# Kernel tuning notes

Measured on AMD Instinct MI355X. Metric: run time of the kernel, lower is better.

Reference implementation:

```python
import jax, jax.numpy as jnp
import numpy as np

N_NODES = 100000
N_EDGES = 3200000
N_FEAT = 128
N_GRAPHS = 256


def setup_inputs() -> dict:
    key = jax.random.key(0)
    ks = jax.random.split(key, 12)
    x = jax.random.normal(ks[0], (N_NODES, N_FEAT), dtype=jnp.float32)
    edge_index = jax.random.randint(ks[1], (2, N_EDGES), 0, N_NODES, dtype=jnp.int64)
    edge_weight = jax.random.uniform(ks[2], (N_EDGES,), dtype=jnp.float32)
    batch = jnp.sort(jax.random.randint(ks[3], (N_NODES,), 0, N_GRAPHS, dtype=jnp.int64))
    def glorot(k, shape):
        lim = np.sqrt(6.0 / (shape[0] + shape[1]))
        return jax.random.uniform(k, shape, dtype=jnp.float32, minval=-lim, maxval=lim)
    W1 = glorot(ks[4], (N_FEAT, 64))
    b1 = jnp.zeros((64,), dtype=jnp.float32)
    W2 = glorot(ks[5], (64, 32))
    b2 = jnp.zeros((32,), dtype=jnp.float32)
    Wl1 = glorot(ks[6], (32, 16))
    bl1 = jnp.zeros((16,), dtype=jnp.float32)
    Wl2 = glorot(ks[7], (16, 1))
    bl2 = jnp.zeros((1,), dtype=jnp.float32)
    return {"x": x, "edge_index": edge_index, "edge_weight": edge_weight,
            "batch": batch, "W1": W1, "b1": b1, "W2": W2, "b2": b2,
            "Wl1": Wl1, "bl1": bl1, "Wl2": Wl2, "bl2": bl2}


def gcn_conv(x, row, col, ew, W, b, num_nodes):
    # x' = D^-1/2 (A + I) D^-1/2 (x W) + b, weights on edges, self-loop weight 1
    h = x @ W  # [N, out]
    deg = jax.ops.segment_sum(ew, col, num_segments=num_nodes) + 1.0  # self-loops add 1
    dinv = jnp.where(deg > 0, jax.lax.rsqrt(deg), 0.0)
    norm = dinv[row] * ew * dinv[col]  # [E]
    msg = h[row] * norm[:, None]  # edge-wise gather + scale
    agg = jax.ops.segment_sum(msg, col, num_segments=num_nodes)
    agg = agg + h * (dinv * dinv)[:, None]  # self-loop contribution
    return agg + b


def reference(x, edge_index, edge_weight, batch, W1, b1, W2, b2, Wl1, bl1, Wl2, bl2):
    row, col = edge_index[0], edge_index[1]
    h = jax.nn.relu(gcn_conv(x, row, col, edge_weight, W1, b1, N_NODES))
    # dropout is identity in eval mode
    h = gcn_conv(h, row, col, edge_weight, W2, b2, N_NODES)
    u = jax.ops.segment_sum(h, batch, num_segments=N_GRAPHS)  # global_add_pool
    out = jax.nn.relu(u @ Wl1 + bl1)
    out = out @ Wl2 + bl2
    return out.reshape(-1)
```

## Files before the change

kernel.cpp:

```cpp
#include <hip/hip_runtime.h>
#include <hip/hip_bf16.h>

#define N_NODES 100000
#define N_EDGES 3200000
#define N_GRAPHS 256

#define NBUCK 391
#define SORT_ITEMS 8192
#define NB_SORT ((N_EDGES + SORT_ITEMS - 1) / SORT_ITEMS)
#define HIST_N (NBUCK * NB_SORT)
#define ROW_MASK 131071

__device__ __forceinline__ float bfl(int d) {
    return __uint_as_float(((unsigned)d) << 16);
}
__device__ __forceinline__ float bfh(int d) {
    return __uint_as_float(((unsigned)d) & 0xffff0000u);
}
__device__ __forceinline__ unsigned short f2bf(float f) {
    __hip_bfloat16 b = __float2bfloat16(f);
    return *(unsigned short*)&b;
}

__global__ __launch_bounds__(512) void hist_kernel(const int* __restrict__ col,
                                                   int* __restrict__ hist) {
    __shared__ int h[NBUCK];
    int tid = threadIdx.x;
    for (int i = tid; i < NBUCK; i += 512) h[i] = 0;
    __syncthreads();
    int base = blockIdx.x * SORT_ITEMS + tid * 4;
    #pragma unroll
    for (int l = 0; l < SORT_ITEMS / 2048; ++l) {
        int e = base + l * 2048;
        if (e < N_EDGES) {
            int4 c4 = *(const int4*)&col[e];
            atomicAdd(&h[c4.x >> 8], 1);
            atomicAdd(&h[c4.y >> 8], 1);
            atomicAdd(&h[c4.z >> 8], 1);
            atomicAdd(&h[c4.w >> 8], 1);
        }
    }
    __syncthreads();
    for (int i = tid; i < NBUCK; i += 512) hist[i * NB_SORT + blockIdx.x] = h[i];
}

__global__ __launch_bounds__(256) void scanA_kernel(int* __restrict__ a,
                                                    int* __restrict__ bsum, int n) {
    __shared__ int s[256];
    int tid = threadIdx.x;
    int base = blockIdx.x * 4096 + tid * 16;
    int v[16];
    int sum = 0;
    #pragma unroll
    for (int i = 0; i < 16; ++i) { v[i] = (base + i < n) ? a[base + i] : 0; sum += v[i]; }
    s[tid] = sum;
    __syncthreads();
    for (int d = 1; d < 256; d <<= 1) {
        int x = (tid >= d) ? s[tid - d] : 0;
        __syncthreads();
        s[tid] += x;
        __syncthreads();
    }
    int run = s[tid] - sum;
    #pragma unroll
    for (int i = 0; i < 16; ++i) {
        if (base + i < n) a[base + i] = run;
        run += v[i];
    }
    if (tid == 255) bsum[blockIdx.x] = s[255];
}

__global__ __launch_bounds__(256) void scanB_kernel(int* bsum, int nb) {
    __shared__ int s[256];
    int tid = threadIdx.x;
    int v = (tid < nb) ? bsum[tid] : 0;
    s[tid] = v;
    __syncthreads();
    for (int d = 1; d < 256; d <<= 1) {
        int x = (tid >= d) ? s[tid - d] : 0;
        __syncthreads();
        s[tid] += x;
        __syncthreads();
    }
    if (tid < nb) bsum[tid] = s[tid] - v;
}

__global__ __launch_bounds__(512) void scatter_sort_kernel(const int* __restrict__ col,
                                                           const int* __restrict__ row,
                                                           const float* __restrict__ ew,
                                                           const int* __restrict__ hist,
                                                           const int* __restrict__ bsum,
                                                           int2* __restrict__ rw2) {
    __shared__ int offs[NBUCK];
    int tid = threadIdx.x;
    for (int i = tid; i < NBUCK; i += 512) {
        int idx = i * NB_SORT + blockIdx.x;
        offs[i] = hist[idx] + bsum[idx >> 12];
    }
    __syncthreads();
    int base = blockIdx.x * SORT_ITEMS + tid * 4;
    #pragma unroll
    for (int l = 0; l < SORT_ITEMS / 2048; ++l) {
        int e = base + l * 2048;
        if (e < N_EDGES) {
            int4 c4 = *(const int4*)&col[e];
            int4 r4 = *(const int4*)&row[e];
            float4 w4 = *(const float4*)&ew[e];
            int p0 = atomicAdd(&offs[c4.x >> 8], 1);
            int p1 = atomicAdd(&offs[c4.y >> 8], 1);
            int p2 = atomicAdd(&offs[c4.z >> 8], 1);
            int p3 = atomicAdd(&offs[c4.w >> 8], 1);
            int2 v0; v0.x = r4.x | ((c4.x & 255) << 17); v0.y = __float_as_int(w4.x);
            int2 v1; v1.x = r4.y | ((c4.y & 255) << 17); v1.y = __float_as_int(w4.y);
            int2 v2; v2.x = r4.z | ((c4.z & 255) << 17); v2.y = __float_as_int(w4.z);
            int2 v3; v3.x = r4.w | ((c4.w & 255) << 17); v3.y = __float_as_int(w4.w);
            rw2[p0] = v0;
            rw2[p1] = v1;
            rw2[p2] = v2;
            rw2[p3] = v3;
        }
    }
}

__global__ __launch_bounds__(256) void build_kernel(const int* __restrict__ hist,
                                                    const int* __restrict__ bsum,
                                                    const int2* __restrict__ rw2,
                                                    int* __restrict__ off,
                                                    int* __restrict__ cnt,
                                                    float* __restrict__ dinv,
                                                    int2* __restrict__ csr) {
    int b = blockIdx.x;
    int tid = threadIdx.x;
    int ib = b * NB_SORT;
    int begin = hist[ib] + bsum[ib >> 12];
    int end = N_EDGES;
    if (b + 1 < NBUCK) {
        int ie = (b + 1) * NB_SORT;
        end = hist[ie] + bsum[ie >> 12];
    }
    __shared__ int lcnt[256];
    __shared__ float ldeg[256];
    __shared__ int s[256];
    __shared__ int curo[256];
    lcnt[tid] = 0;
    ldeg[tid] = 0.f;
    __syncthreads();
    for (int e = begin + tid; e < end; e += 1024) {
        int2 a0 = rw2[e];
        int e1 = e + 256, e2 = e + 512, e3 = e + 768;
        int2 a1 = (e1 < end) ? rw2[e1] : make_int2(0, 0);
        int2 a2 = (e2 < end) ? rw2[e2] : make_int2(0, 0);
        int2 a3 = (e3 < end) ? rw2[e3] : make_int2(0, 0);
        atomicAdd(&lcnt[a0.x >> 17], 1);
        atomicAdd(&ldeg[a0.x >> 17], __int_as_float(a0.y));
        if (e1 < end) { atomicAdd(&lcnt[a1.x >> 17], 1); atomicAdd(&ldeg[a1.x >> 17], __int_as_float(a1.y)); }
        if (e2 < end) { atomicAdd(&lcnt[a2.x >> 17], 1); atomicAdd(&ldeg[a2.x >> 17], __int_as_float(a2.y)); }
        if (e3 < end) { atomicAdd(&lcnt[a3.x >> 17], 1); atomicAdd(&ldeg[a3.x >> 17], __int_as_float(a3.y)); }
    }
    __syncthreads();
    int v = lcnt[tid];
    s[tid] = v;
    __syncthreads();
    for (int d = 1; d < 256; d <<= 1) {
        int x = (tid >= d) ? s[tid - d] : 0;
        __syncthreads();
        s[tid] += x;
        __syncthreads();
    }
    int excl = s[tid] - v;
    int node = (b << 8) + tid;
    if (node < N_NODES) {
        off[node] = begin + excl;
        cnt[node] = v;
        dinv[node] = rsqrtf(1.0f + ldeg[tid]);
    }
    curo[tid] = begin + excl;
    __syncthreads();
    for (int e = begin + tid; e < end; e += 1024) {
        int2 a0 = rw2[e];
        int e1 = e + 256, e2 = e + 512, e3 = e + 768;
        int2 a1 = (e1 < end) ? rw2[e1] : make_int2(0, 0);
        int2 a2 = (e2 < end) ? rw2[e2] : make_int2(0, 0);
        int2 a3 = (e3 < end) ? rw2[e3] : make_int2(0, 0);
        int p0 = atomicAdd(&curo[a0.x >> 17], 1);
        csr[p0] = make_int2(a0.x & ROW_MASK, a0.y);
        if (e1 < end) { int p = atomicAdd(&curo[a1.x >> 17], 1); csr[p] = make_int2(a1.x & ROW_MASK, a1.y); }
        if (e2 < end) { int p = atomicAdd(&curo[a2.x >> 17], 1); csr[p] = make_int2(a2.x & ROW_MASK, a2.y); }
        if (e3 < end) { int p = atomicAdd(&curo[a3.x >> 17], 1); csr[p] = make_int2(a3.x & ROW_MASK, a3.y); }
    }
}

template <int IN, int OUT, int ROWS>
__global__ __launch_bounds__(256) void gemm_bf16_kernel(const float* __restrict__ X,
                                                        const float* __restrict__ W,
                                                        const float* __restrict__ scale,
                                                        unsigned short* __restrict__ H, int n) {
    constexpr int BK = 16;
    constexpr int TX = OUT / 4;
    constexpr int TY = ROWS / 8;
    static_assert(TX * TY == 256, "block must be 256 threads");
    __shared__ float xsT[BK][ROWS + 4];
    __shared__ float ws[BK][OUT + 4];
    int tid = threadIdx.x;
    int tx = tid % TX, ty = tid / TX;
    int r0 = blockIdx.x * ROWS;
    float acc[8][4] = {};
    for (int k0 = 0; k0 < IN; k0 += BK) {
        constexpr int XL = (ROWS * BK) / (256 * 4);
        #pragma unroll
        for (int l = 0; l < XL; ++l) {
            int t = tid + l * 256;
            int rr = t >> 2;
            int kp = (t & 3) * 4;
            float4 v = make_float4(0.f, 0.f, 0.f, 0.f);
            int gr = r0 + rr;
            if (gr < n) v = *(const float4*)&X[(size_t)gr * IN + k0 + kp];
            xsT[kp + 0][rr] = v.x;
            xsT[kp + 1][rr] = v.y;
            xsT[kp + 2][rr] = v.z;
            xsT[kp + 3][rr] = v.w;
        }
        constexpr int WL = (BK * OUT) / 4;
        if (WL == 256 || tid < WL) {
            int kr = tid / TX;
            int cp = (tid % TX) * 4;
            float4 v = *(const float4*)&W[(size_t)(k0 + kr) * OUT + cp];
            *(float4*)&ws[kr][cp] = v;
        }
        __syncthreads();
        #pragma unroll
        for (int kk = 0; kk < BK; ++kk) {
            float4 a0 = *(const float4*)&xsT[kk][ty * 8];
            float4 a1 = *(const float4*)&xsT[kk][ty * 8 + 4];
            float4 b = *(const float4*)&ws[kk][tx * 4];
            float av[8] = {a0.x, a0.y, a0.z, a0.w, a1.x, a1.y, a1.z, a1.w};
            float bv[4] = {b.x, b.y, b.z, b.w};
            #pragma unroll
            for (int i = 0; i < 8; ++i) {
                #pragma unroll
                for (int j = 0; j < 4; ++j) acc[i][j] = fmaf(av[i], bv[j], acc[i][j]);
            }
        }
        __syncthreads();
    }
    #pragma unroll
    for (int i = 0; i < 8; ++i) {
        int gr = r0 + ty * 8 + i;
        if (gr < n) {
            float sc = scale[gr];
            ushort4 o;
            o.x = f2bf(acc[i][0] * sc);
            o.y = f2bf(acc[i][1] * sc);
            o.z = f2bf(acc[i][2] * sc);
            o.w = f2bf(acc[i][3] * sc);
            *(ushort4*)&H[(size_t)gr * OUT + tx * 4] = o;
        }
    }
}

__global__ __launch_bounds__(256) void agg1_kernel(const int2* __restrict__ csr,
                                                   const int* __restrict__ off,
                                                   const int* __restrict__ cnt,
                                                   const float* __restrict__ dinv,
                                                   const unsigned short* __restrict__ h1t,
                                                   const float* __restrict__ b1,
                                                   float* __restrict__ h1p) {
    int lane = threadIdx.x & 63;
    int node = blockIdx.x * 4 + (threadIdx.x >> 6);
    int es = lane >> 3;
    int fb = lane & 7;
    int s = off[node], c = cnt[node];
    float acc[8] = {};
    for (int j0 = 0; j0 < c; j0 += 64) {
        int m = min(64, c - j0);
        int2 e = make_int2(0, 0);
        if (lane < m) e = csr[s + j0 + lane];
        int ng = (m + 7) >> 3;
        int g = 0;
        for (; g + 2 <= ng; g += 2) {
            int s0 = g * 8 + es;
            int s1 = s0 + 8;
            int r0 = __shfl(e.x, s0);
            float w0 = __int_as_float(__shfl(e.y, s0));
            int r1 = __shfl(e.x, s1);
            float w1 = __int_as_float(__shfl(e.y, s1));
            int4 d0 = *(const int4*)(h1t + (((size_t)r0) << 6) + (fb << 3));
            int4 d1 = *(const int4*)(h1t + (((size_t)r1) << 6) + (fb << 3));
            acc[0] = fmaf(w0, bfl(d0.x), acc[0]);
            acc[1] = fmaf(w0, bfh(d0.x), acc[1]);
            acc[2] = fmaf(w0, bfl(d0.y), acc[2]);
            acc[3] = fmaf(w0, bfh(d0.y), acc[3]);
            acc[4] = fmaf(w0, bfl(d0.z), acc[4]);
            acc[5] = fmaf(w0, bfh(d0.z), acc[5]);
            acc[6] = fmaf(w0, bfl(d0.w), acc[6]);
            acc[7] = fmaf(w0, bfh(d0.w), acc[7]);
            acc[0] = fmaf(w1, bfl(d1.x), acc[0]);
            acc[1] = fmaf(w1, bfh(d1.x), acc[1]);
            acc[2] = fmaf(w1, bfl(d1.y), acc[2]);
            acc[3] = fmaf(w1, bfh(d1.y), acc[3]);
            acc[4] = fmaf(w1, bfl(d1.z), acc[4]);
            acc[5] = fmaf(w1, bfh(d1.z), acc[5]);
            acc[6] = fmaf(w1, bfl(d1.w), acc[6]);
            acc[7] = fmaf(w1, bfh(d1.w), acc[7]);
        }
        if (g < ng) {
            int s0 = g * 8 + es;
            int r0 = __shfl(e.x, s0);
            float w0 = __int_as_float(__shfl(e.y, s0));
            int4 d0 = *(const int4*)(h1t + (((size_t)r0) << 6) + (fb << 3));
            acc[0] = fmaf(w0, bfl(d0.x), acc[0]);
            acc[1] = fmaf(w0, bfh(d0.x), acc[1]);
            acc[2] = fmaf(w0, bfl(d0.y), acc[2]);
            acc[3] = fmaf(w0, bfh(d0.y), acc[3]);
            acc[4] = fmaf(w0, bfl(d0.z), acc[4]);
            acc[5] = fmaf(w0, bfh(d0.z), acc[5]);
            acc[6] = fmaf(w0, bfl(d0.w), acc[6]);
            acc[7] = fmaf(w0, bfh(d0.w), acc[7]);
        }
    }
    #pragma unroll
    for (int mask = 8; mask <= 32; mask <<= 1) {
        #pragma unroll
        for (int k = 0; k < 8; ++k) acc[k] += __shfl_xor(acc[k], mask);
    }
    if (es == 0) {
        float di = dinv[node];
        int4 ds = *(const int4*)(h1t + (((size_t)node) << 6) + (fb << 3));
        float4 bv0 = *(const float4*)&b1[fb * 8];
        float4 bv1 = *(const float4*)&b1[fb * 8 + 4];
        float4 o0, o1;
        o0.x = fmaxf(fmaf(acc[0] + bfl(ds.x), di, bv0.x), 0.f);
        o0.y = fmaxf(fmaf(acc[1] + bfh(ds.x), di, bv0.y), 0.f);
        o0.z = fmaxf(fmaf(acc[2] + bfl(ds.y), di, bv0.z), 0.f);
        o0.w = fmaxf(fmaf(acc[3] + bfh(ds.y), di, bv0.w), 0.f);
        o1.x = fmaxf(fmaf(acc[4] + bfl(ds.z), di, bv1.x), 0.f);
        o1.y = fmaxf(fmaf(acc[5] + bfh(ds.z), di, bv1.y), 0.f);
        o1.z = fmaxf(fmaf(acc[6] + bfl(ds.w), di, bv1.z), 0.f);
        o1.w = fmaxf(fmaf(acc[7] + bfh(ds.w), di, bv1.w), 0.f);
        float* po = h1p + (size_t)node * 64 + fb * 8;
        *(float4*)po = o0;
        *(float4*)(po + 4) = o1;
    }
}

__global__ __launch_bounds__(256) void agg2_kernel(const int2* __restrict__ csr,
                                                   const int* __restrict__ off,
                                                   const int* __restrict__ cnt,
                                                   const float* __restrict__ dinv,
                                                   const unsigned short* __restrict__ h2t,
                                                   const float* __restrict__ b2,
                                                   float* __restrict__ h2p) {
    int lane = threadIdx.x & 63;
    int half = lane >> 5;
    int hl = lane & 31;
    int es = hl >> 2;
    int fb = hl & 3;
    int wid = threadIdx.x >> 6;
    int node = blockIdx.x * 8 + wid * 2 + half;
    int s = off[node], c = cnt[node];
    int lbase = half << 5;
    float acc[8] = {};
    for (int j0 = 0; j0 < c; j0 += 32) {
        int m = min(32, c - j0);
        int2 e = make_int2(0, 0);
        if (hl < m) e = csr[s + j0 + hl];
        int ng = (m + 7) >> 3;
        int g = 0;
        for (; g + 2 <= ng; g += 2) {
            int s0 = lbase + g * 8 + es;
            int s1 = s0 + 8;
            int r0 = __shfl(e.x, s0);
            float w0 = __int_as_float(__shfl(e.y, s0));
            int r1 = __shfl(e.x, s1);
            float w1 = __int_as_float(__shfl(e.y, s1));
            int4 d0 = *(const int4*)(h2t + (((size_t)r0) << 5) + (fb << 3));
            int4 d1 = *(const int4*)(h2t + (((size_t)r1) << 5) + (fb << 3));
            acc[0] = fmaf(w0, bfl(d0.x), acc[0]);
            acc[1] = fmaf(w0, bfh(d0.x), acc[1]);
            acc[2] = fmaf(w0, bfl(d0.y), acc[2]);
            acc[3] = fmaf(w0, bfh(d0.y), acc[3]);
            acc[4] = fmaf(w0, bfl(d0.z), acc[4]);
            acc[5] = fmaf(w0, bfh(d0.z), acc[5]);
            acc[6] = fmaf(w0, bfl(d0.w), acc[6]);
            acc[7] = fmaf(w0, bfh(d0.w), acc[7]);
            acc[0] = fmaf(w1, bfl(d1.x), acc[0]);
            acc[1] = fmaf(w1, bfh(d1.x), acc[1]);
            acc[2] = fmaf(w1, bfl(d1.y), acc[2]);
            acc[3] = fmaf(w1, bfh(d1.y), acc[3]);
            acc[4] = fmaf(w1, bfl(d1.z), acc[4]);
            acc[5] = fmaf(w1, bfh(d1.z), acc[5]);
            acc[6] = fmaf(w1, bfl(d1.w), acc[6]);
            acc[7] = fmaf(w1, bfh(d1.w), acc[7]);
        }
        if (g < ng) {
            int s0 = lbase + g * 8 + es;
            int r0 = __shfl(e.x, s0);
            float w0 = __int_as_float(__shfl(e.y, s0));
            int4 d0 = *(const int4*)(h2t + (((size_t)r0) << 5) + (fb << 3));
            acc[0] = fmaf(w0, bfl(d0.x), acc[0]);
            acc[1] = fmaf(w0, bfh(d0.x), acc[1]);
            acc[2] = fmaf(w0, bfl(d0.y), acc[2]);
            acc[3] = fmaf(w0, bfh(d0.y), acc[3]);
            acc[4] = fmaf(w0, bfl(d0.z), acc[4]);
            acc[5] = fmaf(w0, bfh(d0.z), acc[5]);
            acc[6] = fmaf(w0, bfl(d0.w), acc[6]);
            acc[7] = fmaf(w0, bfh(d0.w), acc[7]);
        }
    }
    #pragma unroll
    for (int mask = 4; mask <= 16; mask <<= 1) {
        #pragma unroll
        for (int k = 0; k < 8; ++k) acc[k] += __shfl_xor(acc[k], mask);
    }
    if (es == 0) {
        float di = dinv[node];
        int4 ds = *(const int4*)(h2t + (((size_t)node) << 5) + (fb << 3));
        float4 bv0 = *(const float4*)&b2[fb * 8];
        float4 bv1 = *(const float4*)&b2[fb * 8 + 4];
        float4 o0, o1;
        o0.x = fmaf(acc[0] + bfl(ds.x), di, bv0.x);
        o0.y = fmaf(acc[1] + bfh(ds.x), di, bv0.y);
        o0.z = fmaf(acc[2] + bfl(ds.y), di, bv0.z);
        o0.w = fmaf(acc[3] + bfh(ds.y), di, bv0.w);
        o1.x = fmaf(acc[4] + bfl(ds.z), di, bv1.x);
        o1.y = fmaf(acc[5] + bfh(ds.z), di, bv1.y);
        o1.z = fmaf(acc[6] + bfl(ds.w), di, bv1.z);
        o1.w = fmaf(acc[7] + bfh(ds.w), di, bv1.w);
        float* po = h2p + (size_t)node * 32 + fb * 8;
        *(float4*)po = o0;
        *(float4*)(po + 4) = o1;
    }
}

__global__ __launch_bounds__(256) void pool_kernel(const float* __restrict__ h2p,
                                                   const int* __restrict__ batch,
                                                   float* __restrict__ u) {
    int g = blockIdx.x;
    int lo = 0, hi = N_NODES;
    while (lo < hi) { int m = (lo + hi) >> 1; if (batch[m] < g) lo = m + 1; else hi = m; }
    int start = lo;
    hi = N_NODES;
    while (lo < hi) { int m = (lo + hi) >> 1; if (batch[m] < g + 1) lo = m + 1; else hi = m; }
    int end = lo;
    int f = threadIdx.x & 31, grp = threadIdx.x >> 5;
    float acc = 0.f;
    for (int n = start + grp; n < end; n += 8) acc += h2p[(size_t)n * 32 + f];
    __shared__ float red[8][32];
    red[grp][f] = acc;
    __syncthreads();
    if (threadIdx.x < 32) {
        float sum = 0.f;
        #pragma unroll
        for (int k = 0; k < 8; ++k) sum += red[k][threadIdx.x];
        u[g * 32 + threadIdx.x] = sum;
    }
}

__global__ __launch_bounds__(256) void head_kernel(const float* __restrict__ u,
                                                   const float* __restrict__ Wl1,
                                                   const float* __restrict__ bl1,
                                                   const float* __restrict__ Wl2,
                                                   const float* __restrict__ bl2,
                                                   float* __restrict__ out) {
    int g = threadIdx.x;
    float uu[32];
    #pragma unroll
    for (int k = 0; k < 32; ++k) uu[k] = u[g * 32 + k];
    float o = bl2[0];
    #pragma unroll
    for (int j = 0; j < 16; ++j) {
        float h = bl1[j];
        #pragma unroll
        for (int k = 0; k < 32; ++k) h = fmaf(uu[k], Wl1[k * 16 + j], h);
        o = fmaf(fmaxf(h, 0.f), Wl2[j], o);
    }
    out[g] = o;
}

extern "C" void kernel_launch(void* const* d_in, const int* in_sizes, int n_in,
                              void* d_out, int out_size, void* d_ws, size_t ws_size,
                              hipStream_t stream) {
    const float* x     = (const float*)d_in[0];
    const int*   ei    = (const int*)d_in[1];
    const float* ew    = (const float*)d_in[2];
    const int*   batch = (const int*)d_in[3];
    const float* W1    = (const float*)d_in[4];
    const float* b1    = (const float*)d_in[5];
    const float* W2    = (const float*)d_in[6];
    const float* b2    = (const float*)d_in[7];
    const float* Wl1   = (const float*)d_in[8];
    const float* bl1   = (const float*)d_in[9];
    const float* Wl2   = (const float*)d_in[10];
    const float* bl2   = (const float*)d_in[11];
    float* out = (float*)d_out;

    const int* row = ei;
    const int* col = ei + N_EDGES;

    char* p = (char*)d_ws;
    auto alloc = [&](size_t bytes) {
        char* q = p;
        p += (bytes + 255) & ~(size_t)255;
        return q;
    };
    int*   hist   = (int*)alloc((size_t)HIST_N * 4);
    int*   bsum   = (int*)alloc(1024 * 4);
    int2*  rw2    = (int2*)alloc((size_t)N_EDGES * 8);
    int*   off    = (int*)alloc(N_NODES * 4);
    int*   cnt    = (int*)alloc(N_NODES * 4);
    float* dinv   = (float*)alloc(N_NODES * 4);
    int2*  csr    = (int2*)alloc((size_t)N_EDGES * 8);
    unsigned short* h1t = (unsigned short*)rw2;
    float* h1p    = (float*)alloc((size_t)N_NODES * 64 * 4);
    unsigned short* h2t = (unsigned short*)alloc((size_t)N_NODES * 32 * 2);
    float* h2p    = (float*)alloc((size_t)N_NODES * 32 * 4);
    float* u      = (float*)alloc(N_GRAPHS * 32 * 4);

    const int nbScan = (HIST_N + 4095) / 4096;

    hist_kernel<<<NB_SORT, 512, 0, stream>>>(col, hist);
    scanA_kernel<<<nbScan, 256, 0, stream>>>(hist, bsum, HIST_N);
    scanB_kernel<<<1, 256, 0, stream>>>(bsum, nbScan);
    scatter_sort_kernel<<<NB_SORT, 512, 0, stream>>>(col, row, ew, hist, bsum, rw2);
    build_kernel<<<NBUCK, 256, 0, stream>>>(hist, bsum, rw2, off, cnt, dinv, csr);

    gemm_bf16_kernel<128, 64, 128><<<(N_NODES + 127) / 128, 256, 0, stream>>>(x, W1, dinv, h1t, N_NODES);
    agg1_kernel<<<N_NODES / 4, 256, 0, stream>>>(csr, off, cnt, dinv, h1t, b1, h1p);
    gemm_bf16_kernel<64, 32, 256><<<(N_NODES + 255) / 256, 256, 0, stream>>>(h1p, W2, dinv, h2t, N_NODES);
    agg2_kernel<<<N_NODES / 8, 256, 0, stream>>>(csr, off, cnt, dinv, h2t, b2, h2p);
    pool_kernel<<<N_GRAPHS, 256, 0, stream>>>(h2p, batch, u);
    head_kernel<<<1, 256, 0, stream>>>(u, Wl1, bl1, Wl2, bl2, out);
}
```

Measured before the change: 246.1 us.

## Store layer-1 output in bf16 and widen build kernel to 512 threads

The first aggregation kernel now writes its ReLU output as packed bf16 instead of fp32, and a new GEMM variant reads bf16 input and expands it to float in shared memory. This halves the bytes written by agg1 and read by the second GEMM. Separately, the CSR build kernel runs with 512 threads per bucket, with the scan widened to 512 and only the first 256 threads writing per-node outputs. Rounding layer-1 activations to bf16 adds a small precision loss before the second layer.

```diff
diff --git a/kernel.cpp b/kernel.cpp
--- a/kernel.cpp
+++ b/kernel.cpp
@@ -20,6 +20,9 @@
 __device__ __forceinline__ unsigned short f2bf(float f) {
     __hip_bfloat16 b = __float2bfloat16(f);
     return *(unsigned short*)&b;
+}
+__device__ __forceinline__ unsigned pack2bf(float lo, float hi) {
+    return (unsigned)f2bf(lo) | ((unsigned)f2bf(hi) << 16);
 }
 
 __global__ __launch_bounds__(512) void hist_kernel(const int* __restrict__ col,
@@ -122,7 +125,7 @@
     }
 }
 
-__global__ __launch_bounds__(256) void build_kernel(const int* __restrict__ hist,
+__global__ __launch_bounds__(512) void build_kernel(const int* __restrict__ hist,
                                                     const int* __restrict__ bsum,
                                                     const int2* __restrict__ rw2,
                                                     int* __restrict__ off,
@@ -140,14 +143,13 @@
     }
     __shared__ int lcnt[256];
     __shared__ float ldeg[256];
-    __shared__ int s[256];
+    __shared__ int s[512];
     __shared__ int curo[256];
-    lcnt[tid] = 0;
-    ldeg[tid] = 0.f;
-    __syncthreads();
-    for (int e = begin + tid; e < end; e += 1024) {
+    if (tid < 256) { lcnt[tid] = 0; ldeg[tid] = 0.f; }
+    __syncthreads();
+    for (int e = begin + tid; e < end; e += 2048) {
         int2 a0 = rw2[e];
-        int e1 = e + 256, e2 = e + 512, e3 = e + 768;
+        int e1 = e + 512, e2 = e + 1024, e3 = e + 1536;
         int2 a1 = (e1 < end) ? rw2[e1] : make_int2(0, 0);
         int2 a2 = (e2 < end) ? rw2[e2] : make_int2(0, 0);
         int2 a3 = (e3 < end) ? rw2[e3] : make_int2(0, 0);
@@ -158,27 +160,29 @@
         if (e3 < end) { atomicAdd(&lcnt[a3.x >> 17], 1); atomicAdd(&ldeg[a3.x >> 17], __int_as_float(a3.y)); }
     }
     __syncthreads();
-    int v = lcnt[tid];
+    int v = (tid < 256) ? lcnt[tid] : 0;
     s[tid] = v;
     __syncthreads();
-    for (int d = 1; d < 256; d <<= 1) {
+    for (int d = 1; d < 512; d <<= 1) {
         int x = (tid >= d) ? s[tid - d] : 0;
         __syncthreads();
         s[tid] += x;
         __syncthreads();
     }
-    int excl = s[tid] - v;
-    int node = (b << 8) + tid;
-    if (node < N_NODES) {
-        off[node] = begin + excl;
-        cnt[node] = v;
-        dinv[node] = rsqrtf(1.0f + ldeg[tid]);
-    }
-    curo[tid] = begin + excl;
-    __syncthreads();
-    for (int e = begin + tid; e < end; e += 1024) {
+    if (tid < 256) {
+        int excl = s[tid] - v;
+        int node = (b << 8) + tid;
+        if (node < N_NODES) {
+            off[node] = begin + excl;
+            cnt[node] = v;
+            dinv[node] = rsqrtf(1.0f + ldeg[tid]);
+        }
+        curo[tid] = begin + excl;
+    }
+    __syncthreads();
+    for (int e = begin + tid; e < end; e += 2048) {
         int2 a0 = rw2[e];
-        int e1 = e + 256, e2 = e + 512, e3 = e + 768;
+        int e1 = e + 512, e2 = e + 1024, e3 = e + 1536;
         int2 a1 = (e1 < end) ? rw2[e1] : make_int2(0, 0);
         int2 a2 = (e2 < end) ? rw2[e2] : make_int2(0, 0);
         int2 a3 = (e3 < end) ? rw2[e3] : make_int2(0, 0);
@@ -258,13 +262,84 @@
     }
 }
 
+template <int IN, int OUT, int ROWS>
+__global__ __launch_bounds__(256) void gemm_bf16in_kernel(const unsigned short* __restrict__ X,
+                                                          const float* __restrict__ W,
+                                                          const float* __restrict__ scale,
+                                                          unsigned short* __restrict__ H, int n) {
+    constexpr int BK = 16;
+    constexpr int TX = OUT / 4;
+    constexpr int TY = ROWS / 8;
+    static_assert(TX * TY == 256, "block must be 256 threads");
+    __shared__ float xsT[BK][ROWS + 4];
+    __shared__ float ws[BK][OUT + 4];
+    int tid = threadIdx.x;
+    int tx = tid % TX, ty = tid / TX;
+    int r0 = blockIdx.x * ROWS;
+    float acc[8][4] = {};
+    for (int k0 = 0; k0 < IN; k0 += BK) {
+        constexpr int XL = (ROWS * BK) / (256 * 4);
+        #pragma unroll
+        for (int l = 0; l < XL; ++l) {
+            int t = tid + l * 256;
+            int rr = t >> 2;
+            int kp = (t & 3) * 4;
+            int gr = r0 + rr;
+            float f0 = 0.f, f1 = 0.f, f2 = 0.f, f3 = 0.f;
+            if (gr < n) {
+                ushort4 v = *(const ushort4*)&X[(size_t)gr * IN + k0 + kp];
+                f0 = bfl(v.x); f1 = bfl(v.y); f2 = bfl(v.z); f3 = bfl(v.w);
+            }
+            xsT[kp + 0][rr] = f0;
+            xsT[kp + 1][rr] = f1;
+            xsT[kp + 2][rr] = f2;
+            xsT[kp + 3][rr] = f3;
+        }
+        constexpr int WL = (BK * OUT) / 4;
+        if (WL == 256 || tid < WL) {
+            int kr = tid / TX;
+            int cp = (tid % TX) * 4;
+            float4 v = *(const float4*)&W[(size_t)(k0 + kr) * OUT + cp];
+            *(float4*)&ws[kr][cp] = v;
+        }
+        __syncthreads();
+        #pragma unroll
+        for (int kk = 0; kk < BK; ++kk) {
+            float4 a0 = *(const float4*)&xsT[kk][ty * 8];
+            float4 a1 = *(const float4*)&xsT[kk][ty * 8 + 4];
+            float4 b = *(const float4*)&ws[kk][tx * 4];
+            float av[8] = {a0.x, a0.y, a0.z, a0.w, a1.x, a1.y, a1.z, a1.w};
+            float bv[4] = {b.x, b.y, b.z, b.w};
+            #pragma unroll
+            for (int i = 0; i < 8; ++i) {
+                #pragma unroll
+                for (int j = 0; j < 4; ++j) acc[i][j] = fmaf(av[i], bv[j], acc[i][j]);
+            }
+        }
+        __syncthreads();
+    }
+    #pragma unroll
+    for (int i = 0; i < 8; ++i) {
+        int gr = r0 + ty * 8 + i;
+        if (gr < n) {
+            float sc = scale[gr];
+            ushort4 o;
+            o.x = f2bf(acc[i][0] * sc);
+            o.y = f2bf(acc[i][1] * sc);
+            o.z = f2bf(acc[i][2] * sc);
+            o.w = f2bf(acc[i][3] * sc);
+            *(ushort4*)&H[(size_t)gr * OUT + tx * 4] = o;
+        }
+    }
+}
+
 __global__ __launch_bounds__(256) void agg1_kernel(const int2* __restrict__ csr,
                                                    const int* __restrict__ off,
                                                    const int* __restrict__ cnt,
                                                    const float* __restrict__ dinv,
                                                    const unsigned short* __restrict__ h1t,
                                                    const float* __restrict__ b1,
-                                                   float* __restrict__ h1p) {
+                                                   unsigned short* __restrict__ h1p) {
     int lane = threadIdx.x & 63;
     int node = blockIdx.x * 4 + (threadIdx.x >> 6);
     int es = lane >> 3;
@@ -328,18 +403,20 @@
         int4 ds = *(const int4*)(h1t + (((size_t)node) << 6) + (fb << 3));
         float4 bv0 = *(const float4*)&b1[fb * 8];
         float4 bv1 = *(const float4*)&b1[fb * 8 + 4];
-        float4 o0, o1;
-        o0.x = fmaxf(fmaf(acc[0] + bfl(ds.x), di, bv0.x), 0.f);
-        o0.y = fmaxf(fmaf(acc[1] + bfh(ds.x), di, bv0.y), 0.f);
-        o0.z = fmaxf(fmaf(acc[2] + bfl(ds.y), di, bv0.z), 0.f);
-        o0.w = fmaxf(fmaf(acc[3] + bfh(ds.y), di, bv0.w), 0.f);
-        o1.x = fmaxf(fmaf(acc[4] + bfl(ds.z), di, bv1.x), 0.f);
-        o1.y = fmaxf(fmaf(acc[5] + bfh(ds.z), di, bv1.y), 0.f);
-        o1.z = fmaxf(fmaf(acc[6] + bfl(ds.w), di, bv1.z), 0.f);
-        o1.w = fmaxf(fmaf(acc[7] + bfh(ds.w), di, bv1.w), 0.f);
-        float* po = h1p + (size_t)node * 64 + fb * 8;
-        *(float4*)po = o0;
-        *(float4*)(po + 4) = o1;
+        float v0 = fmaxf(fmaf(acc[0] + bfl(ds.x), di, bv0.x), 0.f);
+        float v1 = fmaxf(fmaf(acc[1] + bfh(ds.x), di, bv0.y), 0.f);
+        float v2 = fmaxf(fmaf(acc[2] + bfl(ds.y), di, bv0.z), 0.f);
+        float v3 = fmaxf(fmaf(acc[3] + bfh(ds.y), di, bv0.w), 0.f);
+        float v4 = fmaxf(fmaf(acc[4] + bfl(ds.z), di, bv1.x), 0.f);
+        float v5 = fmaxf(fmaf(acc[5] + bfh(ds.z), di, bv1.y), 0.f);
+        float v6 = fmaxf(fmaf(acc[6] + bfl(ds.w), di, bv1.z), 0.f);
+        float v7 = fmaxf(fmaf(acc[7] + bfh(ds.w), di, bv1.w), 0.f);
+        int4 o;
+        o.x = (int)pack2bf(v0, v1);
+        o.y = (int)pack2bf(v2, v3);
+        o.z = (int)pack2bf(v4, v5);
+        o.w = (int)pack2bf(v6, v7);
+        *(int4*)(h1p + (size_t)node * 64 + fb * 8) = o;
     }
 }
 
@@ -511,7 +588,7 @@
     float* dinv   = (float*)alloc(N_NODES * 4);
     int2*  csr    = (int2*)alloc((size_t)N_EDGES * 8);
     unsigned short* h1t = (unsigned short*)rw2;
-    float* h1p    = (float*)alloc((size_t)N_NODES * 64 * 4);
+    unsigned short* h1p = (unsigned short*)alloc((size_t)N_NODES * 64 * 2);
     unsigned short* h2t = (unsigned short*)alloc((size_t)N_NODES * 32 * 2);
     float* h2p    = (float*)alloc((size_t)N_NODES * 32 * 4);
     float* u      = (float*)alloc(N_GRAPHS * 32 * 4);
@@ -522,11 +599,11 @@
     scanA_kernel<<<nbScan, 256, 0, stream>>>(hist, bsum, HIST_N);
     scanB_kernel<<<1, 256, 0, stream>>>(bsum, nbScan);
     scatter_sort_kernel<<<NB_SORT, 512, 0, stream>>>(col, row, ew, hist, bsum, rw2);
-    build_kernel<<<NBUCK, 256, 0, stream>>>(hist, bsum, rw2, off, cnt, dinv, csr);
+    build_kernel<<<NBUCK, 512, 0, stream>>>(hist, bsum, rw2, off, cnt, dinv, csr);
 
     gemm_bf16_kernel<128, 64, 128><<<(N_NODES + 127) / 128, 256, 0, stream>>>(x, W1, dinv, h1t, N_NODES);
     agg1_kernel<<<N_NODES / 4, 256, 0, stream>>>(csr, off, cnt, dinv, h1t, b1, h1p);
-    gemm_bf16_kernel<64, 32, 256><<<(N_NODES + 255) / 256, 256, 0, stream>>>(h1p, W2, dinv, h2t, N_NODES);
+    gemm_bf16in_kernel<64, 32, 256><<<(N_NODES + 255) / 256, 256, 0, stream>>>(h1p, W2, dinv, h2t, N_NODES);
     agg2_kernel<<<N_NODES / 8, 256, 0, stream>>>(csr, off, cnt, dinv, h2t, b2, h2p);
     pool_kernel<<<N_GRAPHS, 256, 0, stream>>>(h2p, batch, u);
     head_kernel<<<1, 256, 0, stream>>>(u, Wl1, bl1, Wl2, bl2, out);
```

Measured after the change: 245.3 us. Within noise of the previous version (-0.3%).

## Fuse second GEMM into layer-1 aggregation and merge pool with head

Applied to the files above, without the earlier changes.

The layer-1 aggregation kernel now applies bias and ReLU, multiplies by W2 in registers, reduces across lanes with shuffles, and writes the dinv-scaled bf16 layer-2 input directly. This removes the fp32 h1p round trip and a separate GEMM launch. The pooling and MLP head kernels are merged into one, and the CSR build kernel moves to 512 threads per block. The cost is extra per-lane register use for the W2 slice and more shuffle work in agg1.

```diff
diff --git a/kernel.cpp b/kernel.cpp
--- a/kernel.cpp
+++ b/kernel.cpp
@@ -20,6 +20,9 @@
 __device__ __forceinline__ unsigned short f2bf(float f) {
     __hip_bfloat16 b = __float2bfloat16(f);
     return *(unsigned short*)&b;
+}
+__device__ __forceinline__ unsigned pack2bf(float lo, float hi) {
+    return (unsigned)f2bf(lo) | ((unsigned)f2bf(hi) << 16);
 }
 
 __global__ __launch_bounds__(512) void hist_kernel(const int* __restrict__ col,
@@ -122,7 +125,7 @@
     }
 }
 
-__global__ __launch_bounds__(256) void build_kernel(const int* __restrict__ hist,
+__global__ __launch_bounds__(512) void build_kernel(const int* __restrict__ hist,
                                                     const int* __restrict__ bsum,
                                                     const int2* __restrict__ rw2,
                                                     int* __restrict__ off,
@@ -140,14 +143,13 @@
     }
     __shared__ int lcnt[256];
     __shared__ float ldeg[256];
-    __shared__ int s[256];
+    __shared__ int s[512];
     __shared__ int curo[256];
-    lcnt[tid] = 0;
-    ldeg[tid] = 0.f;
-    __syncthreads();
-    for (int e = begin + tid; e < end; e += 1024) {
+    if (tid < 256) { lcnt[tid] = 0; ldeg[tid] = 0.f; }
+    __syncthreads();
+    for (int e = begin + tid; e < end; e += 2048) {
         int2 a0 = rw2[e];
-        int e1 = e + 256, e2 = e + 512, e3 = e + 768;
+        int e1 = e + 512, e2 = e + 1024, e3 = e + 1536;
         int2 a1 = (e1 < end) ? rw2[e1] : make_int2(0, 0);
         int2 a2 = (e2 < end) ? rw2[e2] : make_int2(0, 0);
         int2 a3 = (e3 < end) ? rw2[e3] : make_int2(0, 0);
@@ -158,27 +160,29 @@
         if (e3 < end) { atomicAdd(&lcnt[a3.x >> 17], 1); atomicAdd(&ldeg[a3.x >> 17], __int_as_float(a3.y)); }
     }
     __syncthreads();
-    int v = lcnt[tid];
+    int v = (tid < 256) ? lcnt[tid] : 0;
     s[tid] = v;
     __syncthreads();
-    for (int d = 1; d < 256; d <<= 1) {
+    for (int d = 1; d < 512; d <<= 1) {
         int x = (tid >= d) ? s[tid - d] : 0;
         __syncthreads();
         s[tid] += x;
         __syncthreads();
     }
-    int excl = s[tid] - v;
-    int node = (b << 8) + tid;
-    if (node < N_NODES) {
-        off[node] = begin + excl;
-        cnt[node] = v;
-        dinv[node] = rsqrtf(1.0f + ldeg[tid]);
-    }
-    curo[tid] = begin + excl;
-    __syncthreads();
-    for (int e = begin + tid; e < end; e += 1024) {
+    if (tid < 256) {
+        int excl = s[tid] - v;
+        int node = (b << 8) + tid;
+        if (node < N_NODES) {
+            off[node] = begin + excl;
+            cnt[node] = v;
+            dinv[node] = rsqrtf(1.0f + ldeg[tid]);
+        }
+        curo[tid] = begin + excl;
+    }
+    __syncthreads();
+    for (int e = begin + tid; e < end; e += 2048) {
         int2 a0 = rw2[e];
-        int e1 = e + 256, e2 = e + 512, e3 = e + 768;
+        int e1 = e + 512, e2 = e + 1024, e3 = e + 1536;
         int2 a1 = (e1 < end) ? rw2[e1] : make_int2(0, 0);
         int2 a2 = (e2 < end) ? rw2[e2] : make_int2(0, 0);
         int2 a3 = (e3 < end) ? rw2[e3] : make_int2(0, 0);
@@ -264,11 +268,18 @@
                                                    const float* __restrict__ dinv,
                                                    const unsigned short* __restrict__ h1t,
                                                    const float* __restrict__ b1,
-                                                   float* __restrict__ h1p) {
+                                                   const float* __restrict__ W2g,
+                                                   unsigned short* __restrict__ h2t) {
     int lane = threadIdx.x & 63;
     int node = blockIdx.x * 4 + (threadIdx.x >> 6);
     int es = lane >> 3;
     int fb = lane & 7;
+    float w2r[8][4];
+    #pragma unroll
+    for (int i = 0; i < 8; ++i) {
+        float4 t = *(const float4*)&W2g[(fb * 8 + i) * 32 + es * 4];
+        w2r[i][0] = t.x; w2r[i][1] = t.y; w2r[i][2] = t.z; w2r[i][3] = t.w;
+    }
     int s = off[node], c = cnt[node];
     float acc[8] = {};
     for (int j0 = 0; j0 < c; j0 += 64) {
@@ -323,23 +334,38 @@
         #pragma unroll
         for (int k = 0; k < 8; ++k) acc[k] += __shfl_xor(acc[k], mask);
     }
-    if (es == 0) {
-        float di = dinv[node];
-        int4 ds = *(const int4*)(h1t + (((size_t)node) << 6) + (fb << 3));
-        float4 bv0 = *(const float4*)&b1[fb * 8];
-        float4 bv1 = *(const float4*)&b1[fb * 8 + 4];
-        float4 o0, o1;
-        o0.x = fmaxf(fmaf(acc[0] + bfl(ds.x), di, bv0.x), 0.f);
-        o0.y = fmaxf(fmaf(acc[1] + bfh(ds.x), di, bv0.y), 0.f);
-        o0.z = fmaxf(fmaf(acc[2] + bfl(ds.y), di, bv0.z), 0.f);
-        o0.w = fmaxf(fmaf(acc[3] + bfh(ds.y), di, bv0.w), 0.f);
-        o1.x = fmaxf(fmaf(acc[4] + bfl(ds.z), di, bv1.x), 0.f);
-        o1.y = fmaxf(fmaf(acc[5] + bfh(ds.z), di, bv1.y), 0.f);
-        o1.z = fmaxf(fmaf(acc[6] + bfl(ds.w), di, bv1.z), 0.f);
-        o1.w = fmaxf(fmaf(acc[7] + bfh(ds.w), di, bv1.w), 0.f);
-        float* po = h1p + (size_t)node * 64 + fb * 8;
-        *(float4*)po = o0;
-        *(float4*)(po + 4) = o1;
+    float di = dinv[node];
+    int4 ds = *(const int4*)(h1t + (((size_t)node) << 6) + (fb << 3));
+    float4 bv0 = *(const float4*)&b1[fb * 8];
+    float4 bv1 = *(const float4*)&b1[fb * 8 + 4];
+    float hp[8];
+    hp[0] = fmaxf(fmaf(acc[0] + bfl(ds.x), di, bv0.x), 0.f);
+    hp[1] = fmaxf(fmaf(acc[1] + bfh(ds.x), di, bv0.y), 0.f);
+    hp[2] = fmaxf(fmaf(acc[2] + bfl(ds.y), di, bv0.z), 0.f);
+    hp[3] = fmaxf(fmaf(acc[3] + bfh(ds.y), di, bv0.w), 0.f);
+    hp[4] = fmaxf(fmaf(acc[4] + bfl(ds.z), di, bv1.x), 0.f);
+    hp[5] = fmaxf(fmaf(acc[5] + bfh(ds.z), di, bv1.y), 0.f);
+    hp[6] = fmaxf(fmaf(acc[6] + bfl(ds.w), di, bv1.z), 0.f);
+    hp[7] = fmaxf(fmaf(acc[7] + bfh(ds.w), di, bv1.w), 0.f);
+    float p0 = 0.f, p1 = 0.f, p2 = 0.f, p3 = 0.f;
+    #pragma unroll
+    for (int i = 0; i < 8; ++i) {
+        p0 = fmaf(hp[i], w2r[i][0], p0);
+        p1 = fmaf(hp[i], w2r[i][1], p1);
+        p2 = fmaf(hp[i], w2r[i][2], p2);
+        p3 = fmaf(hp[i], w2r[i][3], p3);
+    }
+    #pragma unroll
+    for (int mask = 1; mask <= 4; mask <<= 1) {
+        p0 += __shfl_xor(p0, mask);
+        p1 += __shfl_xor(p1, mask);
+        p2 += __shfl_xor(p2, mask);
+        p3 += __shfl_xor(p3, mask);
+    }
+    if (fb == 0) {
+        unsigned lo = pack2bf(p0 * di, p1 * di);
+        unsigned hi = pack2bf(p2 * di, p3 * di);
+        *(int2*)(h2t + (((size_t)node) << 5) + (es << 2)) = make_int2((int)lo, (int)hi);
     }
 }
 
@@ -432,9 +458,13 @@
     }
 }
 
-__global__ __launch_bounds__(256) void pool_kernel(const float* __restrict__ h2p,
-                                                   const int* __restrict__ batch,
-                                                   float* __restrict__ u) {
+__global__ __launch_bounds__(256) void pool_head_kernel(const float* __restrict__ h2p,
+                                                        const int* __restrict__ batch,
+                                                        const float* __restrict__ Wl1,
+                                                        const float* __restrict__ bl1,
+                                                        const float* __restrict__ Wl2,
+                                                        const float* __restrict__ bl2,
+                                                        float* __restrict__ out) {
     int g = blockIdx.x;
     int lo = 0, hi = N_NODES;
     while (lo < hi) { int m = (lo + hi) >> 1; if (batch[m] < g) lo = m + 1; else hi = m; }
@@ -446,35 +476,28 @@
     float acc = 0.f;
     for (int n = start + grp; n < end; n += 8) acc += h2p[(size_t)n * 32 + f];
     __shared__ float red[8][32];
+    __shared__ float usum[32];
     red[grp][f] = acc;
     __syncthreads();
     if (threadIdx.x < 32) {
         float sum = 0.f;
         #pragma unroll
         for (int k = 0; k < 8; ++k) sum += red[k][threadIdx.x];
-        u[g * 32 + threadIdx.x] = sum;
-    }
-}
-
-__global__ __launch_bounds__(256) void head_kernel(const float* __restrict__ u,
-                                                   const float* __restrict__ Wl1,
-                                                   const float* __restrict__ bl1,
-                                                   const float* __restrict__ Wl2,
-                                                   const float* __restrict__ bl2,
-                                                   float* __restrict__ out) {
-    int g = threadIdx.x;
-    float uu[32];
-    #pragma unroll
-    for (int k = 0; k < 32; ++k) uu[k] = u[g * 32 + k];
-    float o = bl2[0];
-    #pragma unroll
-    for (int j = 0; j < 16; ++j) {
+        usum[threadIdx.x] = sum;
+    }
+    __syncthreads();
+    if (threadIdx.x < 16) {
+        int j = threadIdx.x;
         float h = bl1[j];
         #pragma unroll
-        for (int k = 0; k < 32; ++k) h = fmaf(uu[k], Wl1[k * 16 + j], h);
-        o = fmaf(fmaxf(h, 0.f), Wl2[j], o);
-    }
-    out[g] = o;
+        for (int k = 0; k < 32; ++k) h = fmaf(usum[k], Wl1[k * 16 + j], h);
+        float t = fmaxf(h, 0.f) * Wl2[j];
+        t += __shfl_xor(t, 1);
+        t += __shfl_xor(t, 2);
+        t += __shfl_xor(t, 4);
+        t += __shfl_xor(t, 8);
+        if (j == 0) out[g] = t + bl2[0];
+    }
 }
 
 extern "C" void kernel_launch(void* const* d_in, const int* in_sizes, int n_in,
@@ -511,10 +534,8 @@
     float* dinv   = (float*)alloc(N_NODES * 4);
     int2*  csr    = (int2*)alloc((size_t)N_EDGES * 8);
     unsigned short* h1t = (unsigned short*)rw2;
-    float* h1p    = (float*)alloc((size_t)N_NODES * 64 * 4);
     unsigned short* h2t = (unsigned short*)alloc((size_t)N_NODES * 32 * 2);
     float* h2p    = (float*)alloc((size_t)N_NODES * 32 * 4);
-    float* u      = (float*)alloc(N_GRAPHS * 32 * 4);
 
     const int nbScan = (HIST_N + 4095) / 4096;
 
@@ -522,12 +543,10 @@
     scanA_kernel<<<nbScan, 256, 0, stream>>>(hist, bsum, HIST_N);
     scanB_kernel<<<1, 256, 0, stream>>>(bsum, nbScan);
     scatter_sort_kernel<<<NB_SORT, 512, 0, stream>>>(col, row, ew, hist, bsum, rw2);
-    build_kernel<<<NBUCK, 256, 0, stream>>>(hist, bsum, rw2, off, cnt, dinv, csr);
+    build_kernel<<<NBUCK, 512, 0, stream>>>(hist, bsum, rw2, off, cnt, dinv, csr);
 
     gemm_bf16_kernel<128, 64, 128><<<(N_NODES + 127) / 128, 256, 0, stream>>>(x, W1, dinv, h1t, N_NODES);
-    agg1_kernel<<<N_NODES / 4, 256, 0, stream>>>(csr, off, cnt, dinv, h1t, b1, h1p);
-    gemm_bf16_kernel<64, 32, 256><<<(N_NODES + 255) / 256, 256, 0, stream>>>(h1p, W2, dinv, h2t, N_NODES);
+    agg1_kernel<<<N_NODES / 4, 256, 0, stream>>>(csr, off, cnt, dinv, h1t, b1, W2, h2t);
     agg2_kernel<<<N_NODES / 8, 256, 0, stream>>>(csr, off, cnt, dinv, h2t, b2, h2p);
-    pool_kernel<<<N_GRAPHS, 256, 0, stream>>>(h2p, batch, u);
-    head_kernel<<<1, 256, 0, stream>>>(u, Wl1, bl1, Wl2, bl2, out);
-}
+    pool_head_kernel<<<N_GRAPHS, 256, 0, stream>>>(h2p, batch, Wl1, bl1, Wl2, bl2, out);
+}
```

New measurement: 300.7 us. 1.22x slower.
